# Kernel tuning notes

Hardware: AMD Instinct MI355X
Metric: run time of the kernel (lower is better)

The kernel has to match this reference:

```python
import jax, jax.numpy as jnp
import numpy as np


def setup_inputs() -> dict:
    key = jax.random.key(0)
    ks = jax.random.split(key, 5)
    B, S, D, O = 8, 2048, 1024, 1024
    q = jax.random.normal(ks[0], (B, S, D), dtype=jnp.float32)
    k = jax.random.normal(ks[1], (B, S, D), dtype=jnp.float32)
    # glorot-scale weights
    scale = (2.0 / (D + O)) ** 0.5
    Wq = jax.random.normal(ks[2], (D, O), dtype=jnp.float32) * scale
    Wk = jax.random.normal(ks[3], (D, O), dtype=jnp.float32) * scale
    Wv = jax.random.normal(ks[4], (D, O), dtype=jnp.float32) * scale
    return {"q": q, "k": k, "Wq": Wq, "Wk": Wk, "Wv": Wv}


def reference(q, k, Wq, Wk, Wv):
    # q: [B, S, Dq], k: [B, S, Dk]
    q_proj = jnp.einsum('bsd,do->bso', q, Wq)   # [B, S, O]
    k_proj = jnp.einsum('bsd,do->bso', k, Wk)   # [B, S, O]
    v_proj = jnp.einsum('bsd,do->bso', k, Wv)   # [B, S, O]
    # Dot(axes=-1): contract feature dims -> [B, Sq, Sk]; NO 1/sqrt(d) scaling
    attn = jnp.einsum('bqo,bko->bqk', q_proj, k_proj)
    attn_w = jax.nn.softmax(attn, axis=-1)      # softmax over key axis
    # Dot(axes=1): contracts the QUERY axis of attn with the seq axis of v (attn^T @ v)
    context = jnp.einsum('bqk,bqo->bko', attn_w, v_proj)  # [B, S, O]
    return jnp.concatenate([q, context], axis=-1)  # [B, S, Dq + O]
```

## Files before the change

kernel.cpp:

```cpp
#include <hip/hip_runtime.h>
#include <hip/hip_bf16.h>


typedef __attribute__((ext_vector_type(4))) float f32x4;
typedef __attribute__((ext_vector_type(16))) float f32x16;
typedef _Float16 f16;
typedef __attribute__((ext_vector_type(8))) _Float16 f16x8;
typedef __attribute__((ext_vector_type(4))) _Float16 f16x4;

#define LOG2E 1.4426950408889634f

#define CM_F32     0
#define CM_F16     1
#define CM_F16T    3
#define CM_ATTN    4
#define CM_PROJ3   5

#define STAGE(WHICH, KS, KT, BO) do { \
    const char* _gb = (WHICH) ? Bb : Ab; \
    const int _ld = (WHICH) ? ldb : lda; \
    const long _r = (WHICH) ? (long)(bn + srow0) : (long)(bm + srow0); \
    const int _k0 = (KT) * 64 + (KS) * 32 + sh8; \
    char* _dst = (char*)smem + (BO) + (WHICH) * 32768 + (KS) * 16384 + wave * 1024; \
    const char* _g0 = _gb + ((_r * _ld + _k0) << 1); \
    const char* _g1 = _gb + (((_r + 128) * _ld + _k0) << 1); \
    __builtin_amdgcn_global_load_lds((const __attribute__((address_space(1))) void*)_g0, \
        (__attribute__((address_space(3))) void*)_dst, 16, 0, 0); \
    __builtin_amdgcn_global_load_lds((const __attribute__((address_space(1))) void*)_g1, \
        (__attribute__((address_space(3))) void*)(_dst + 8192), 16, 0, 0); \
} while (0)

#define GPHASE2(KS, STAGE_CODE, VM) do { \
    f16x8 af[2][4], bb[2][2]; \
    _Pragma("unroll") \
    for (int s = 0; s < 2; ++s) { \
        _Pragma("unroll") \
        for (int mt = 0; mt < 4; ++mt) \
            af[s][mt] = *(const f16x8*)(smem + \
                ((bufo + (KS) * 16384 + abase[mt]) ^ (s << 5))); \
        _Pragma("unroll") \
        for (int nt = 0; nt < 2; ++nt) \
            bb[s][nt] = *(const f16x8*)(smem + \
                ((bufo + (KS) * 16384 + bbase[nt]) ^ (s << 5))); \
    } \
    STAGE_CODE; \
    __builtin_amdgcn_s_barrier(); \
    __builtin_amdgcn_s_setprio(1); \
    _Pragma("unroll") \
    for (int s = 0; s < 2; ++s) \
        _Pragma("unroll") \
        for (int mt = 0; mt < 4; ++mt) \
            _Pragma("unroll") \
            for (int nt = 0; nt < 2; ++nt) \
                acc[mt][nt] = __builtin_amdgcn_mfma_f32_32x32x16_f16( \
                    af[s][mt], bb[s][nt], acc[mt][nt], 0, 0, 0); \
    __builtin_amdgcn_s_setprio(0); \
    VM; \
    __builtin_amdgcn_s_barrier(); \
} while (0)

template<int CMODE>
__global__ __launch_bounds__(512, 2)
void gemm256(const f16* __restrict__ A, const f16* __restrict__ B,
             void* __restrict__ Cv,
             int M, int N, int K, int lda, int ldb, int ldc,
             long az, long bz, long cz,
             float* __restrict__ pm, float* __restrict__ ps)
{
    __shared__ __align__(16) char smem[131072];

    const int z = blockIdx.z;
    const char* Ab;
    const char* Bb;
    if (CMODE == CM_PROJ3) {
        const int y = blockIdx.y;
        Ab = (const char*)(A + (y ? (long)M * 1024 : 0));
        Bb = (const char*)(B + (long)y * 1024 * 1024);
    } else {
        Ab = (const char*)(A + z * az);
        Bb = (const char*)(B + z * bz);
    }

    const int nbx = N >> 8;
    int wg = blockIdx.x;
    const int nwg = gridDim.x;
    if ((nwg & 7) == 0) wg = (wg & 7) * (nwg >> 3) + (wg >> 3);
    const int bm = (wg / nbx) << 8;
    const int bn = (wg % nbx) << 8;

    const int tid = threadIdx.x;
    const int wave = tid >> 6;
    const int lane = tid & 63;
    const int l31 = lane & 31;
    const int h5 = lane >> 5;
    const int wm = wave >> 2;
    const int wn = wave & 3;

    const int f3 = (l31 ^ (l31 >> 2)) & 3;
    const int sl = ((h5 ^ f3) << 4);
    int abase[4], bbase[2];
    #pragma unroll
    for (int mt = 0; mt < 4; ++mt)
        abase[mt] = (wm * 128 + mt * 32 + l31) * 64 + sl;
    #pragma unroll
    for (int nt = 0; nt < 2; ++nt)
        bbase[nt] = 32768 + (wn * 64 + nt * 32 + l31) * 64 + sl;

    const int srow0 = tid >> 2;
    const int sh8 = ((tid ^ (tid >> 2) ^ (tid >> 4)) & 3) * 8;

    f32x16 acc[4][2];
    #pragma unroll
    for (int mt = 0; mt < 4; ++mt)
        #pragma unroll
        for (int nt = 0; nt < 2; ++nt)
            acc[mt][nt] = (f32x16)(0.f);

    const int nt_k = K >> 6;

    {
        const int t1p = (nt_k > 1) ? 1 : 0;
        STAGE(0, 0, 0, 0);
        STAGE(1, 0, 0, 0);
        STAGE(0, 1, 0, 0);
        STAGE(1, 1, 0, 0);
        STAGE(0, 0, t1p, 65536);
        STAGE(1, 0, t1p, 65536);
        asm volatile("s_waitcnt vmcnt(4)" ::: "memory");
        __builtin_amdgcn_s_barrier();
    }

    for (int t = 0; t < nt_k; ++t) {
        const int bufo = (t & 1) << 16;
        const int nbo = bufo ^ 65536;
        const int t1 = (t + 1 < nt_k) ? t + 1 : nt_k - 1;
        const int t2 = (t + 2 < nt_k) ? t + 2 : nt_k - 1;
        GPHASE2(0, { STAGE(0, 1, t1, nbo); STAGE(1, 1, t1, nbo); },
                asm volatile("s_waitcnt vmcnt(8)" ::: "memory"));
        GPHASE2(1, { STAGE(0, 0, t2, bufo); STAGE(1, 0, t2, bufo); },
                asm volatile("s_waitcnt vmcnt(8)" ::: "memory"));
    }
    asm volatile("s_waitcnt vmcnt(0)" ::: "memory");

    if (CMODE == CM_ATTN) {
        f16* E = (f16*)Cv + z * cz;
        #pragma unroll
        for (int nt = 0; nt < 2; ++nt) {
            float Mx = -3.4e38f;
            #pragma unroll
            for (int mt = 0; mt < 4; ++mt)
                #pragma unroll
                for (int r = 0; r < 16; ++r)
                    Mx = fmaxf(Mx, acc[mt][nt][r]);
            Mx = fmaxf(Mx, __shfl_xor(Mx, 32, 64));
            float Sm = 0.f;
            #pragma unroll
            for (int mt = 0; mt < 4; ++mt)
                #pragma unroll
                for (int r = 0; r < 16; ++r) {
                    const float e = exp2f((acc[mt][nt][r] - Mx) * LOG2E);
                    acc[mt][nt][r] = e;
                    Sm += e;
                }
            Sm += __shfl_xor(Sm, 32, 64);
            const int col = bn + wn * 64 + nt * 32 + l31;
            #pragma unroll
            for (int mt = 0; mt < 4; ++mt) {
                const int row0 = bm + wm * 128 + mt * 32 + h5 * 4;
                #pragma unroll
                for (int rq = 0; rq < 4; ++rq)
                    #pragma unroll
                    for (int rr = 0; rr < 4; ++rr)
                        E[(long)(row0 + rq * 8 + rr) * ldc + col] =
                            (f16)acc[mt][nt][rq * 4 + rr];
            }
            if (lane < 32) {
                const long pidx = ((long)z * 16 + (bm >> 7) + wm) * N + col;
                pm[pidx] = Mx * LOG2E;
                ps[pidx] = Sm;
            }
        }
        return;
    }

    #pragma unroll
    for (int mt = 0; mt < 4; ++mt) {
        #pragma unroll
        for (int nt = 0; nt < 2; ++nt) {
            const int row0 = bm + wm * 128 + mt * 32 + h5 * 4;
            const int col = bn + wn * 64 + nt * 32 + l31;
            if (CMODE == CM_F32) {
                float* C = (float*)Cv + z * cz;
                #pragma unroll
                for (int rq = 0; rq < 4; ++rq)
                    #pragma unroll
                    for (int rr = 0; rr < 4; ++rr)
                        C[(long)(row0 + rq * 8 + rr) * ldc + col] =
                            acc[mt][nt][rq * 4 + rr];
            } else if (CMODE == CM_F16) {
                f16* C = (f16*)Cv + z * cz;
                #pragma unroll
                for (int rq = 0; rq < 4; ++rq)
                    #pragma unroll
                    for (int rr = 0; rr < 4; ++rr)
                        C[(long)(row0 + rq * 8 + rr) * ldc + col] =
                            (f16)acc[mt][nt][rq * 4 + rr];
            } else if (CMODE == CM_F16T) {
                f16* C = (f16*)Cv + z * cz;
                #pragma unroll
                for (int rq = 0; rq < 4; ++rq) {
                    f16x4 v;
                    #pragma unroll
                    for (int rr = 0; rr < 4; ++rr) v[rr] = (f16)acc[mt][nt][rq * 4 + rr];
                    *(f16x4*)(C + (long)col * ldc + row0 + rq * 8) = v;
                }
            } else {
                const int y = blockIdx.y;
                if (y < 2) {
                    f16* C = (f16*)Cv + (long)y * M * 1024;
                    #pragma unroll
                    for (int rq = 0; rq < 4; ++rq)
                        #pragma unroll
                        for (int rr = 0; rr < 4; ++rr)
                            C[(long)(row0 + rq * 8 + rr) * 1024 + col] =
                                (f16)acc[mt][nt][rq * 4 + rr];
                } else {
                    f16* C = (f16*)pm;
                    #pragma unroll
                    for (int rq = 0; rq < 4; ++rq) {
                        f16x4 v;
                        #pragma unroll
                        for (int rr = 0; rr < 4; ++rr)
                            v[rr] = (f16)acc[mt][nt][rq * 4 + rr];
                        *(f16x4*)(C + (long)col * M + row0 + rq * 8) = v;
                    }
                }
            }
        }
    }
}

__global__ __launch_bounds__(256)
void pack_cast_q(const float* __restrict__ in, f16* __restrict__ op,
                 float* __restrict__ oq, long nquads)
{
    const long i = (long)blockIdx.x * 256 + threadIdx.x;
    if (i >= nquads) return;
    const long row = i >> 8;
    const int c = (int)(i & 255) * 4;
    const float4 v = *(const float4*)(in + row * 1024 + c);
    *(float4*)(oq + row * 2048 + c) = v;
    f16x4 h;
    h[0] = (f16)v.x; h[1] = (f16)v.y; h[2] = (f16)v.z; h[3] = (f16)v.w;
    *(f16x4*)(op + row * 1024 + c) = h;
}

__global__ __launch_bounds__(256)
void pack_cast_k(const float* __restrict__ in, f16* __restrict__ op, long nquads)
{
    const long i = (long)blockIdx.x * 256 + threadIdx.x;
    if (i >= nquads) return;
    const long row = i >> 8;
    const int c = (int)(i & 255) * 4;
    const float4 v = *(const float4*)(in + row * 1024 + c);
    f16x4 h;
    h[0] = (f16)v.x; h[1] = (f16)v.y; h[2] = (f16)v.z; h[3] = (f16)v.w;
    *(f16x4*)(op + row * 1024 + c) = h;
}

__global__ __launch_bounds__(256)
void pack_W_T(const float* __restrict__ W, f16* __restrict__ Wt)
{
    __shared__ float tile[64][65];
    const int d0 = blockIdx.y * 64, o0 = blockIdx.x * 64;
    const int t = threadIdx.x;
    const int rr = t >> 4, c4 = (t & 15) * 4;
    #pragma unroll
    for (int it = 0; it < 4; ++it) {
        const int r = rr + it * 16;
        const float4 v = *(const float4*)(W + (long)(d0 + r) * 1024 + o0 + c4);
        tile[r][c4] = v.x; tile[r][c4 + 1] = v.y;
        tile[r][c4 + 2] = v.z; tile[r][c4 + 3] = v.w;
    }
    __syncthreads();
    #pragma unroll
    for (int it = 0; it < 4; ++it) {
        const int orow = rr + it * 16;
        f16x4 h;
        #pragma unroll
        for (int j = 0; j < 4; ++j) h[j] = (f16)tile[c4 + j][orow];
        *(f16x4*)(Wt + (long)(o0 + orow) * 1024 + d0 + c4) = h;
    }
}

__global__ __launch_bounds__(256)
void softmax_merge16(const float* __restrict__ pm, const float* __restrict__ ps,
                     float* __restrict__ scale, int nq)
{
    const int idx = blockIdx.x * 256 + threadIdx.x;
    if (idx >= nq) return;
    const int z = idx >> 11, q = idx & 2047;
    const float* pmz = pm + ((long)z * 16) * 2048 + q;
    const float* psz = ps + ((long)z * 16) * 2048 + q;
    float mx = -3.4e38f;
    #pragma unroll
    for (int j = 0; j < 16; ++j) mx = fmaxf(mx, pmz[j * 2048]);
    float s = 0.f;
    #pragma unroll
    for (int j = 0; j < 16; ++j)
        s += psz[j * 2048] * exp2f(pmz[j * 2048] - mx);
    const float L = mx + log2f(s);
    float* sc = scale + ((long)z * 16) * 2048 + q;
    #pragma unroll
    for (int j = 0; j < 16; ++j)
        sc[j * 2048] = exp2f(pmz[j * 2048] - L);
}

__global__ __launch_bounds__(256)
void rescale_e(f16* __restrict__ e, const float* __restrict__ scale, long n8)
{
    const long idx = (long)blockIdx.x * 256 + threadIdx.x;
    if (idx >= n8) return;
    const long z = idx >> 19;
    const int within = (int)(idx & ((1 << 19) - 1));
    const int kk = within >> 8;
    const int q8 = (within & 255) * 8;
    const float* sc = scale + ((long)z * 16 + (kk >> 7)) * 2048 + q8;
    const float4 s0 = *(const float4*)sc;
    const float4 s1 = *(const float4*)(sc + 4);
    f16x8 v = *(f16x8*)(e + idx * 8);
    v[0] = (f16)((float)v[0] * s0.x); v[1] = (f16)((float)v[1] * s0.y);
    v[2] = (f16)((float)v[2] * s0.z); v[3] = (f16)((float)v[3] * s0.w);
    v[4] = (f16)((float)v[4] * s1.x); v[5] = (f16)((float)v[5] * s1.y);
    v[6] = (f16)((float)v[6] * s1.z); v[7] = (f16)((float)v[7] * s1.w);
    *(f16x8*)(e + idx * 8) = v;
}

__global__ __launch_bounds__(256)
void copy_q_kernel(const float* __restrict__ q, float* __restrict__ out, long n4)
{
    const long idx = (long)blockIdx.x * 256 + threadIdx.x;
    if (idx >= n4) return;
    const long row = idx >> 8;
    const long c4 = idx & 255;
    *(float4*)(&out[row * 2048 + c4 * 4]) =
        *(const float4*)(&q[row * 1024 + c4 * 4]);
}

#define BM 64
#define BN 64
#define BKF 16
template<int opA, int opB>
__global__ __launch_bounds__(256)
void sgemm(const float* __restrict__ A, const float* __restrict__ B,
           float* __restrict__ C,
           int M, int N, int K, int lda, int ldb, int ldc)
{
    __shared__ float As[BKF][BM];
    __shared__ float Bs[BKF][BN];
    const int tid = threadIdx.x;
    const int tx = tid & 15, ty = tid >> 4;
    const int bm = blockIdx.y * BM, bn = blockIdx.x * BN;
    float acc[4][4] = {};
    for (int k0 = 0; k0 < K; k0 += BKF) {
        if (opA == 0) {
            const int row = tid >> 2, kq = (tid & 3) * 4;
            const float4 v = *(const float4*)(A + (long)(bm + row) * lda + (k0 + kq));
            As[kq + 0][row] = v.x; As[kq + 1][row] = v.y;
            As[kq + 2][row] = v.z; As[kq + 3][row] = v.w;
        } else {
            const int kk = tid >> 4, mq = (tid & 15) * 4;
            *(float4*)(&As[kk][mq]) =
                *(const float4*)(A + (long)(k0 + kk) * lda + (bm + mq));
        }
        if (opB == 0) {
            const int kk = tid >> 4, nq = (tid & 15) * 4;
            *(float4*)(&Bs[kk][nq]) =
                *(const float4*)(B + (long)(k0 + kk) * ldb + (bn + nq));
        } else {
            const int row = tid >> 2, kq = (tid & 3) * 4;
            const float4 v = *(const float4*)(B + (long)(bn + row) * ldb + (k0 + kq));
            Bs[kq + 0][row] = v.x; Bs[kq + 1][row] = v.y;
            Bs[kq + 2][row] = v.z; Bs[kq + 3][row] = v.w;
        }
        __syncthreads();
        #pragma unroll
        for (int kk = 0; kk < BKF; ++kk) {
            const float4 a = *(const float4*)(&As[kk][ty * 4]);
            const float4 b = *(const float4*)(&Bs[kk][tx * 4]);
            const float av[4] = {a.x, a.y, a.z, a.w};
            const float bv[4] = {b.x, b.y, b.z, b.w};
            #pragma unroll
            for (int i = 0; i < 4; ++i)
                #pragma unroll
                for (int j = 0; j < 4; ++j)
                    acc[i][j] += av[i] * bv[j];
        }
        __syncthreads();
    }
    #pragma unroll
    for (int i = 0; i < 4; ++i) {
        const float4 v = make_float4(acc[i][0], acc[i][1], acc[i][2], acc[i][3]);
        *(float4*)(&C[(long)(bm + ty * 4 + i) * ldc + (bn + tx * 4)]) = v;
    }
}

__device__ __forceinline__ float wave_reduce_max(float v) {
    #pragma unroll
    for (int off = 1; off < 64; off <<= 1)
        v = fmaxf(v, __shfl_xor(v, off, 64));
    return v;
}
__device__ __forceinline__ float wave_reduce_sum(float v) {
    #pragma unroll
    for (int off = 1; off < 64; off <<= 1)
        v += __shfl_xor(v, off, 64);
    return v;
}

__global__ __launch_bounds__(256)
void softmax_rows2048(float* __restrict__ X)
{
    float* x = X + (long)blockIdx.x * 2048;
    const int tid = threadIdx.x;
    float4 v0 = *(const float4*)(&x[tid * 4]);
    float4 v1 = *(const float4*)(&x[1024 + tid * 4]);
    float m = fmaxf(fmaxf(fmaxf(v0.x, v0.y), fmaxf(v0.z, v0.w)),
                    fmaxf(fmaxf(v1.x, v1.y), fmaxf(v1.z, v1.w)));
    m = wave_reduce_max(m);
    __shared__ float sm[4];
    __shared__ float ss[4];
    const int wid = tid >> 6;
    if ((tid & 63) == 0) sm[wid] = m;
    __syncthreads();
    m = fmaxf(fmaxf(sm[0], sm[1]), fmaxf(sm[2], sm[3]));
    v0.x = expf(v0.x - m); v0.y = expf(v0.y - m);
    v0.z = expf(v0.z - m); v0.w = expf(v0.w - m);
    v1.x = expf(v1.x - m); v1.y = expf(v1.y - m);
    v1.z = expf(v1.z - m); v1.w = expf(v1.w - m);
    float s = (v0.x + v0.y + v0.z + v0.w) + (v1.x + v1.y + v1.z + v1.w);
    s = wave_reduce_sum(s);
    if ((tid & 63) == 0) ss[wid] = s;
    __syncthreads();
    s = ss[0] + ss[1] + ss[2] + ss[3];
    const float inv = 1.0f / s;
    v0.x *= inv; v0.y *= inv; v0.z *= inv; v0.w *= inv;
    v1.x *= inv; v1.y *= inv; v1.z *= inv; v1.w *= inv;
    *(float4*)(&x[tid * 4]) = v0;
    *(float4*)(&x[1024 + tid * 4]) = v1;
}

static void fallback_fp32(const float* q, const float* k, const float* Wq,
                          const float* Wk, const float* Wv, float* out,
                          void* d_ws, hipStream_t stream)
{
    const int S = 2048, D = 1024, O = 1024, B = 8;
    float* qp = (float*)d_ws;
    float* kp = qp + (size_t)S * O;
    float* vp = kp + (size_t)S * O;
    float* attn = vp + (size_t)S * O;
    const long n4 = (long)B * S * D / 4;
    copy_q_kernel<<<dim3((n4 + 255) / 256), 256, 0, stream>>>(q, out, n4);
    const dim3 blk(256);
    const dim3 gproj(O / BN, S / BM), gattn(S / BN, S / BM), gctx(O / BN, S / BM);
    for (int b = 0; b < B; ++b) {
        const float* qb = q + (size_t)b * S * D;
        const float* kb = k + (size_t)b * S * D;
        float* outc = out + (size_t)b * S * 2048 + D;
        sgemm<0, 0><<<gproj, blk, 0, stream>>>(qb, Wq, qp, S, O, D, D, O, O);
        sgemm<0, 0><<<gproj, blk, 0, stream>>>(kb, Wk, kp, S, O, D, D, O, O);
        sgemm<0, 0><<<gproj, blk, 0, stream>>>(kb, Wv, vp, S, O, D, D, O, O);
        sgemm<0, 1><<<gattn, blk, 0, stream>>>(qp, kp, attn, S, S, O, O, O, S);
        softmax_rows2048<<<dim3(S), blk, 0, stream>>>(attn);
        sgemm<1, 0><<<gctx, blk, 0, stream>>>(attn, vp, outc, S, O, S, S, O, 2048);
    }
}

extern "C" void kernel_launch(void* const* d_in, const int* in_sizes, int n_in,
                              void* d_out, int out_size, void* d_ws, size_t ws_size,
                              hipStream_t stream)
{
    const float* q  = (const float*)d_in[0];
    const float* k  = (const float*)d_in[1];
    const float* Wq = (const float*)d_in[2];
    const float* Wk = (const float*)d_in[3];
    const float* Wv = (const float*)d_in[4];
    float* out = (float*)d_out;

    const int B = 8, S = 2048;

    auto need = [](int g) -> size_t {
        const size_t wpk = 3 * (size_t)1024 * 1024 * 2;
        const size_t pkA = (size_t)g * 2048 * 1024 * 2;
        const size_t vpT = (size_t)1024 * g * 2048 * 2;
        const size_t aw  = (size_t)g * 2048 * 2048 * 2;
        const size_t pp  = 3 * (size_t)g * 16 * 2048 * 4;
        return wpk + 4 * pkA + vpT + aw + pp + 32 * 256;
    };
    int g = 0;
    for (int cand : {8, 4, 2, 1})
        if (need(cand) <= ws_size) { g = cand; break; }
    if (g == 0) { fallback_fp32(q, k, Wq, Wk, Wv, out, d_ws, stream); return; }

    char* p = (char*)d_ws;
    auto carve = [&](size_t bytes) {
        char* r = p;
        p += (bytes + 255) & ~(size_t)255;
        return r;
    };
    f16* Wtq = (f16*)carve((size_t)1024 * 1024 * 2);
    f16* Wtk = (f16*)carve((size_t)1024 * 1024 * 2);
    f16* Wtv = (f16*)carve((size_t)1024 * 1024 * 2);
    const size_t pkAB = (size_t)g * 2048 * 1024 * 2;
    f16* qpack   = (f16*)carve(pkAB);
    f16* kpack   = (f16*)carve(pkAB);
    f16* qp_pack = (f16*)carve(pkAB);
    f16* kp_pack = (f16*)carve(pkAB);
    f16* vpT     = (f16*)carve((size_t)1024 * g * 2048 * 2);
    f16* attn_w  = (f16*)carve((size_t)g * 2048 * 2048 * 2);
    float* pmb   = (float*)carve((size_t)g * 16 * 2048 * 4);
    float* psb   = (float*)carve((size_t)g * 16 * 2048 * 4);
    float* scb   = (float*)carve((size_t)g * 16 * 2048 * 4);

    pack_W_T<<<dim3(16, 16), 256, 0, stream>>>(Wq, Wtq);
    pack_W_T<<<dim3(16, 16), 256, 0, stream>>>(Wk, Wtk);
    pack_W_T<<<dim3(16, 16), 256, 0, stream>>>(Wv, Wtv);

    const int Mg = g * 2048;
    const dim3 blk(256);
    const dim3 blk512(512);
    const long zSS = (long)2048 * 2048;
    const long zSD = (long)2048 * 1024;

    for (int gi = 0; gi < B / g; ++gi) {
        const float* qg = q + (size_t)gi * Mg * 1024;
        const float* kg = k + (size_t)gi * Mg * 1024;
        float* outq = out + (size_t)gi * Mg * 2048;

        const long nquads = (long)Mg * 256;
        pack_cast_q<<<dim3((nquads + 255) / 256), blk, 0, stream>>>(
            qg, qpack, outq, nquads);
        pack_cast_k<<<dim3((nquads + 255) / 256), blk, 0, stream>>>(
            kg, kpack, nquads);

        const dim3 g1((1024 / 256) * (Mg / 256), 3, 1);
        gemm256<CM_PROJ3><<<g1, blk512, 0, stream>>>(
            qpack, Wtq, qp_pack, Mg, 1024, 1024, 1024, 1024, 1024, 0, 0, 0,
            (float*)vpT, nullptr);

        const dim3 g2((2048 / 256) * (2048 / 256), 1, g);
        gemm256<CM_ATTN><<<g2, blk512, 0, stream>>>(
            kp_pack, qp_pack, attn_w, 2048, 2048, 1024, 1024, 1024, 2048,
            zSD, zSD, zSS, pmb, psb);

        const int nq = g * 2048;
        softmax_merge16<<<dim3((nq + 255) / 256), blk, 0, stream>>>(pmb, psb, scb, nq);
        const long n8 = (long)g * 2048 * 256;
        rescale_e<<<dim3((n8 + 255) / 256), blk, 0, stream>>>(attn_w, scb, n8);

        float* outg = out + (size_t)gi * Mg * 2048 + 1024;
        const dim3 g3((1024 / 256) * (2048 / 256), 1, g);
        gemm256<CM_F32><<<g3, blk512, 0, stream>>>(
            attn_w, vpT, outg, 2048, 1024, 2048, 2048, Mg, 2048,
            zSS, 2048, zSS, nullptr, nullptr);
    }
}
```

Baseline: 377.7 us.

## Fuse softmax rescale into PV GEMM A-operand load; merge q/k cast kernels

Removes the standalone rescale_e pass over the g×2048×2048 fp16 attention matrix. The per-(key-block, query) softmax scale is now stored as fp16, staged into extra LDS inside the PV GEMM, and multiplied into the A fragments before each MFMA. This trades one full read/write of the attention matrix for extra LDS and VALU multiplies in the GEMM inner loop. The diff also merges the q and k cast kernels into one launch and changes the vmcnt waits in the pipelined loop. The larger LDS footprint (139264 bytes per block) may reduce occupancy, and rounding the scale to fp16 adds some numeric error.

```diff
diff --git a/kernel.cpp b/kernel.cpp
--- a/kernel.cpp
+++ b/kernel.cpp
@@ -15,6 +15,7 @@
 #define CM_F16T    3
 #define CM_ATTN    4
 #define CM_PROJ3   5
+#define CM_PVS     6
 
 #define STAGE(WHICH, KS, KT, BO) do { \
     const char* _gb = (WHICH) ? Bb : Ab; \
@@ -31,7 +32,7 @@
 } while (0)
 
 #define GPHASE2(KS, STAGE_CODE, VM) do { \
-    f16x8 af[2][4], bb[2][2]; \
+    f16x8 af[2][4], bb[2][2], sv[2]; \
     _Pragma("unroll") \
     for (int s = 0; s < 2; ++s) { \
         _Pragma("unroll") \
@@ -42,9 +43,19 @@
         for (int nt = 0; nt < 2; ++nt) \
             bb[s][nt] = *(const f16x8*)(smem + \
                 ((bufo + (KS) * 16384 + bbase[nt]) ^ (s << 5))); \
+        if (CMODE == CM_PVS) \
+            sv[s] = *(const f16x8*)(smem + 131072 + wm * 4096 + \
+                t * 128 + (KS) * 64 + s * 32 + (h5 << 4)); \
     } \
     STAGE_CODE; \
     __builtin_amdgcn_s_barrier(); \
+    if (CMODE == CM_PVS) { \
+        _Pragma("unroll") \
+        for (int s = 0; s < 2; ++s) \
+            _Pragma("unroll") \
+            for (int mt = 0; mt < 4; ++mt) \
+                af[s][mt] *= sv[s]; \
+    } \
     __builtin_amdgcn_s_setprio(1); \
     _Pragma("unroll") \
     for (int s = 0; s < 2; ++s) \
@@ -67,7 +78,7 @@
              long az, long bz, long cz,
              float* __restrict__ pm, float* __restrict__ ps)
 {
-    __shared__ __align__(16) char smem[131072];
+    __shared__ __align__(16) char smem[139264];
 
     const int z = blockIdx.z;
     const char* Ab;
@@ -119,6 +130,14 @@
     const int nt_k = K >> 6;
 
     {
+        if (CMODE == CM_PVS) {
+            const char* gsc = (const char*)ps +
+                (((long)z * 16 + (bm >> 7)) * 2048) * 2 + tid * 16;
+            __builtin_amdgcn_global_load_lds(
+                (const __attribute__((address_space(1))) void*)gsc,
+                (__attribute__((address_space(3))) void*)
+                    ((char*)smem + 131072 + wave * 1024), 16, 0, 0);
+        }
         const int t1p = (nt_k > 1) ? 1 : 0;
         STAGE(0, 0, 0, 0);
         STAGE(1, 0, 0, 0);
@@ -135,10 +154,9 @@
         const int nbo = bufo ^ 65536;
         const int t1 = (t + 1 < nt_k) ? t + 1 : nt_k - 1;
         const int t2 = (t + 2 < nt_k) ? t + 2 : nt_k - 1;
-        GPHASE2(0, { STAGE(0, 1, t1, nbo); STAGE(1, 1, t1, nbo); },
-                asm volatile("s_waitcnt vmcnt(8)" ::: "memory"));
+        GPHASE2(0, { STAGE(0, 1, t1, nbo); STAGE(1, 1, t1, nbo); }, );
         GPHASE2(1, { STAGE(0, 0, t2, bufo); STAGE(1, 0, t2, bufo); },
-                asm volatile("s_waitcnt vmcnt(8)" ::: "memory"));
+                asm volatile("s_waitcnt vmcnt(4)" ::: "memory"));
     }
     asm volatile("s_waitcnt vmcnt(0)" ::: "memory");
 
@@ -189,7 +207,7 @@
         for (int nt = 0; nt < 2; ++nt) {
             const int row0 = bm + wm * 128 + mt * 32 + h5 * 4;
             const int col = bn + wn * 64 + nt * 32 + l31;
-            if (CMODE == CM_F32) {
+            if (CMODE == CM_F32 || CMODE == CM_PVS) {
                 float* C = (float*)Cv + z * cz;
                 #pragma unroll
                 for (int rq = 0; rq < 4; ++rq)
@@ -241,31 +259,26 @@
 }
 
 __global__ __launch_bounds__(256)
-void pack_cast_q(const float* __restrict__ in, f16* __restrict__ op,
-                 float* __restrict__ oq, long nquads)
+void pack_cast_qk(const float* __restrict__ qin, const float* __restrict__ kin,
+                  f16* __restrict__ qp, f16* __restrict__ kp,
+                  float* __restrict__ oq, long nquads)
 {
     const long i = (long)blockIdx.x * 256 + threadIdx.x;
-    if (i >= nquads) return;
-    const long row = i >> 8;
-    const int c = (int)(i & 255) * 4;
-    const float4 v = *(const float4*)(in + row * 1024 + c);
-    *(float4*)(oq + row * 2048 + c) = v;
+    if (i >= 2 * nquads) return;
+    const int isK = (i >= nquads);
+    const long j = isK ? i - nquads : i;
+    const long row = j >> 8;
+    const int c = (int)(j & 255) * 4;
+    const float4 v = isK ? *(const float4*)(kin + row * 1024 + c)
+                         : *(const float4*)(qin + row * 1024 + c);
     f16x4 h;
     h[0] = (f16)v.x; h[1] = (f16)v.y; h[2] = (f16)v.z; h[3] = (f16)v.w;
-    *(f16x4*)(op + row * 1024 + c) = h;
-}
-
-__global__ __launch_bounds__(256)
-void pack_cast_k(const float* __restrict__ in, f16* __restrict__ op, long nquads)
-{
-    const long i = (long)blockIdx.x * 256 + threadIdx.x;
-    if (i >= nquads) return;
-    const long row = i >> 8;
-    const int c = (int)(i & 255) * 4;
-    const float4 v = *(const float4*)(in + row * 1024 + c);
-    f16x4 h;
-    h[0] = (f16)v.x; h[1] = (f16)v.y; h[2] = (f16)v.z; h[3] = (f16)v.w;
-    *(f16x4*)(op + row * 1024 + c) = h;
+    if (isK) {
+        *(f16x4*)(kp + row * 1024 + c) = h;
+    } else {
+        *(float4*)(oq + row * 2048 + c) = v;
+        *(f16x4*)(qp + row * 1024 + c) = h;
+    }
 }
 
 __global__ __launch_bounds__(256)
@@ -295,7 +308,7 @@
 
 __global__ __launch_bounds__(256)
 void softmax_merge16(const float* __restrict__ pm, const float* __restrict__ ps,
-                     float* __restrict__ scale, int nq)
+                     f16* __restrict__ scale, int nq)
 {
     const int idx = blockIdx.x * 256 + threadIdx.x;
     if (idx >= nq) return;
@@ -310,30 +323,10 @@
     for (int j = 0; j < 16; ++j)
         s += psz[j * 2048] * exp2f(pmz[j * 2048] - mx);
     const float L = mx + log2f(s);
-    float* sc = scale + ((long)z * 16) * 2048 + q;
+    f16* sc = scale + ((long)z * 16) * 2048 + q;
     #pragma unroll
     for (int j = 0; j < 16; ++j)
-        sc[j * 2048] = exp2f(pmz[j * 2048] - L);
-}
-
-__global__ __launch_bounds__(256)
-void rescale_e(f16* __restrict__ e, const float* __restrict__ scale, long n8)
-{
-    const long idx = (long)blockIdx.x * 256 + threadIdx.x;
-    if (idx >= n8) return;
-    const long z = idx >> 19;
-    const int within = (int)(idx & ((1 << 19) - 1));
-    const int kk = within >> 8;
-    const int q8 = (within & 255) * 8;
-    const float* sc = scale + ((long)z * 16 + (kk >> 7)) * 2048 + q8;
-    const float4 s0 = *(const float4*)sc;
-    const float4 s1 = *(const float4*)(sc + 4);
-    f16x8 v = *(f16x8*)(e + idx * 8);
-    v[0] = (f16)((float)v[0] * s0.x); v[1] = (f16)((float)v[1] * s0.y);
-    v[2] = (f16)((float)v[2] * s0.z); v[3] = (f16)((float)v[3] * s0.w);
-    v[4] = (f16)((float)v[4] * s1.x); v[5] = (f16)((float)v[5] * s1.y);
-    v[6] = (f16)((float)v[6] * s1.z); v[7] = (f16)((float)v[7] * s1.w);
-    *(f16x8*)(e + idx * 8) = v;
+        sc[j * 2048] = (f16)exp2f(pmz[j * 2048] - L);
 }
 
 __global__ __launch_bounds__(256)
@@ -494,7 +487,7 @@
         const size_t pkA = (size_t)g * 2048 * 1024 * 2;
         const size_t vpT = (size_t)1024 * g * 2048 * 2;
         const size_t aw  = (size_t)g * 2048 * 2048 * 2;
-        const size_t pp  = 3 * (size_t)g * 16 * 2048 * 4;
+        const size_t pp  = 2 * (size_t)g * 16 * 2048 * 4 + (size_t)g * 16 * 2048 * 2;
         return wpk + 4 * pkA + vpT + aw + pp + 32 * 256;
     };
     int g = 0;
@@ -520,7 +513,7 @@
     f16* attn_w  = (f16*)carve((size_t)g * 2048 * 2048 * 2);
     float* pmb   = (float*)carve((size_t)g * 16 * 2048 * 4);
     float* psb   = (float*)carve((size_t)g * 16 * 2048 * 4);
-    float* scb   = (float*)carve((size_t)g * 16 * 2048 * 4);
+    f16* scb     = (f16*)carve((size_t)g * 16 * 2048 * 2);
 
     pack_W_T<<<dim3(16, 16), 256, 0, stream>>>(Wq, Wtq);
     pack_W_T<<<dim3(16, 16), 256, 0, stream>>>(Wk, Wtk);
@@ -538,10 +531,8 @@
         float* outq = out + (size_t)gi * Mg * 2048;
 
         const long nquads = (long)Mg * 256;
-        pack_cast_q<<<dim3((nquads + 255) / 256), blk, 0, stream>>>(
-            qg, qpack, outq, nquads);
-        pack_cast_k<<<dim3((nquads + 255) / 256), blk, 0, stream>>>(
-            kg, kpack, nquads);
+        pack_cast_qk<<<dim3((2 * nquads + 255) / 256), blk, 0, stream>>>(
+            qg, kg, qpack, kpack, outq, nquads);
 
         const dim3 g1((1024 / 256) * (Mg / 256), 3, 1);
         gemm256<CM_PROJ3><<<g1, blk512, 0, stream>>>(
@@ -555,13 +546,11 @@
 
         const int nq = g * 2048;
         softmax_merge16<<<dim3((nq + 255) / 256), blk, 0, stream>>>(pmb, psb, scb, nq);
-        const long n8 = (long)g * 2048 * 256;
-        rescale_e<<<dim3((n8 + 255) / 256), blk, 0, stream>>>(attn_w, scb, n8);
 
         float* outg = out + (size_t)gi * Mg * 2048 + 1024;
         const dim3 g3((1024 / 256) * (2048 / 256), 1, g);
-        gemm256<CM_F32><<<g3, blk512, 0, stream>>>(
+        gemm256<CM_PVS><<<g3, blk512, 0, stream>>>(
             attn_w, vpT, outg, 2048, 1024, 2048, 2048, Mg, 2048,
-            zSS, 2048, zSS, nullptr, nullptr);
-    }
-}
+            zSS, 2048, zSS, nullptr, (float*)scb);
+    }
+}
```

Result: faster. 362.1 us (-4.1%).
